# Kernel optimization log

Measured on AMD Instinct MI355X. Metric: run time of the kernel, lower is better.

The kernel has to match this reference:

```python
import jax, jax.numpy as jnp
import numpy as np

HEAD_DIM = 64
NUM_Q_HEADS = 32
NUM_KV_HEADS = 8
ROPE_FREQ = 10000.0
EPS = 1e-6


def _rms_norm(x, gamma):
    # normalize over last dim (head_dim)
    var = jnp.mean(jnp.square(x), axis=-1, keepdims=True)
    return x * jax.lax.rsqrt(var + EPS) * gamma


def _rope_cos_sin(seq_len, dtype=jnp.float32):
    inv_freq = 1.0 / (ROPE_FREQ ** (jnp.arange(0, HEAD_DIM, 2, dtype=jnp.float32) / HEAD_DIM))
    pos = jnp.arange(seq_len, dtype=jnp.float32)
    freqs = pos[:, None] * inv_freq[None, :]          # [S, hd/2]
    emb = jnp.concatenate([freqs, freqs], axis=-1)    # [S, hd]
    return jnp.cos(emb).astype(dtype), jnp.sin(emb).astype(dtype)


def _rotate_half(x):
    x1, x2 = jnp.split(x, 2, axis=-1)
    return jnp.concatenate([-x2, x1], axis=-1)


def _apply_rope(x, cos, sin):
    # x: [B, H, S, hd]; cos/sin: [S, hd]
    return x * cos[None, None, :, :] + _rotate_half(x) * sin[None, None, :, :]


def setup_inputs() -> dict:
    key = jax.random.key(0)
    ks = jax.random.split(key, 5)
    B, S, D = 2, 2048, 2048
    qkv_out = (NUM_Q_HEADS + 2 * NUM_KV_HEADS) * HEAD_DIM  # 3072
    x = jax.random.normal(ks[0], (B, S, D), dtype=jnp.float32)
    w_qkv = jax.random.normal(ks[1], (qkv_out, D), dtype=jnp.float32) * (D ** -0.5)
    w_out = jax.random.normal(ks[2], (D, NUM_Q_HEADS * HEAD_DIM), dtype=jnp.float32) * ((NUM_Q_HEADS * HEAD_DIM) ** -0.5)
    q_gamma = jnp.ones((HEAD_DIM,), dtype=jnp.float32)
    k_gamma = jnp.ones((HEAD_DIM,), dtype=jnp.float32)
    return {"x": x, "w_qkv": w_qkv, "w_out": w_out, "q_gamma": q_gamma, "k_gamma": k_gamma}


def reference(x, w_qkv, w_out, q_gamma, k_gamma):
    B, S, D = x.shape
    groups = NUM_Q_HEADS // NUM_KV_HEADS
    # fused QKV projection (no bias)
    qkv = jnp.einsum("bsd,od->bso", x, w_qkv)
    qkv = qkv.reshape(B, S, NUM_Q_HEADS + 2 * NUM_KV_HEADS, HEAD_DIM)
    qkv = jnp.transpose(qkv, (0, 2, 1, 3))  # [B, heads, S, hd]
    q = qkv[:, :NUM_Q_HEADS]
    k = qkv[:, NUM_Q_HEADS:NUM_Q_HEADS + NUM_KV_HEADS]
    v = qkv[:, NUM_Q_HEADS + NUM_KV_HEADS:]
    # QK RMSNorm over head_dim
    q = _rms_norm(q, q_gamma)
    k = _rms_norm(k, k_gamma)
    # RoPE
    cos, sin = _rope_cos_sin(S, dtype=x.dtype)
    q = _apply_rope(q, cos, sin)
    k = _apply_rope(k, cos, sin)
    # GQA: repeat-interleave kv heads
    k = jnp.repeat(k, groups, axis=1)
    v = jnp.repeat(v, groups, axis=1)
    # causal SDPA
    scale = HEAD_DIM ** -0.5
    scores = jnp.einsum("bhqd,bhkd->bhqk", q, k) * scale
    causal = jnp.tril(jnp.ones((S, S), dtype=bool))
    scores = jnp.where(causal[None, None], scores, jnp.finfo(scores.dtype).min)
    attn = jax.nn.softmax(scores, axis=-1)
    ctx = jnp.einsum("bhqk,bhkd->bhqd", attn, v)
    ctx = jnp.transpose(ctx, (0, 2, 1, 3)).reshape(B, S, NUM_Q_HEADS * HEAD_DIM)
    out = jnp.einsum("bsf,df->bsd", ctx, w_out)
    return out
```

## Files before the change

### kernel.cpp

```cpp
#include <hip/hip_runtime.h>

typedef _Float16 f16;
typedef __fp16 fp16x2 __attribute__((ext_vector_type(2)));
typedef _Float16 f16x8 __attribute__((ext_vector_type(8)));
typedef float f32x4 __attribute__((ext_vector_type(4)));
typedef float f32x16 __attribute__((ext_vector_type(16)));

#define AS1 __attribute__((address_space(1)))
#define AS3 __attribute__((address_space(3)))

#define SCALE_L2E 0.18033688011112042f


__device__ __forceinline__ void gload16(const void* g, void* l) {
    __builtin_amdgcn_global_load_lds(
        (const AS1 unsigned*)(unsigned long long)g,
        (AS3 unsigned*)(unsigned)(unsigned long long)l,
        16, 0, 0);
}

__device__ __forceinline__ unsigned pk2(float a, float b) {
    union { fp16x2 v; unsigned u; } c;
    c.v = __builtin_amdgcn_cvt_pkrtz(a, b);
    return c.u;
}

#define BAR() do { asm volatile("" ::: "memory"); __builtin_amdgcn_s_barrier(); asm volatile("" ::: "memory"); } while (0)


__global__ __launch_bounds__(256) void k_cast(const float* __restrict__ in,
                                              f16* __restrict__ out, int n) {
    int i = (blockIdx.x * 256 + threadIdx.x) * 4;
    if (i + 3 < n) {
        float4 v = *(const float4*)(in + i);
        union { f16 h[4]; ushort4 u; } c;
        c.h[0] = (f16)v.x; c.h[1] = (f16)v.y; c.h[2] = (f16)v.z; c.h[3] = (f16)v.w;
        *(ushort4*)(out + i) = c.u;
    }
}


__global__ __launch_bounds__(256) void k_tab(float* __restrict__ cosT,
                                             float* __restrict__ sinT) {
    int idx = blockIdx.x * 256 + threadIdx.x;
    int s = idx >> 5, i = idx & 31;
    float ang = (float)s * exp2f(-(float)i * 0.4152410118609190f);
    cosT[idx] = cosf(ang);
    sinT[idx] = sinf(ang);
}


#define STG_A(t, h) do { \
    gload16(gA + (size_t)((h) * 128) * K + (t) * 64,      sm + (((t) & 1) * 65536) + (h) * 16384 + tid * 16); \
    gload16(gA + (size_t)((h) * 128 + 64) * K + (t) * 64, sm + (((t) & 1) * 65536) + (h) * 16384 + 8192 + tid * 16); \
} while (0)
#define STG_B(t, h) do { \
    gload16(gB + (size_t)((h) * 128) * K + (t) * 64,      sm + (((t) & 1) * 65536) + 32768 + (h) * 16384 + tid * 16); \
    gload16(gB + (size_t)((h) * 128 + 64) * K + (t) * 64, sm + (((t) & 1) * 65536) + 32768 + (h) * 16384 + 8192 + tid * 16); \
} while (0)

template <typename OutT>
__global__ __launch_bounds__(512, 2) void k_gemm256(const f16* __restrict__ A,
                                                    const f16* __restrict__ Bt,
                                                    OutT* __restrict__ C,
                                                    int M, int N, int K) {
    __shared__ __align__(16) char sm[131072];
    const int tid = threadIdx.x;
    const int lane = tid & 63, wid = tid >> 6;
    const int wm = wid >> 2, wn = wid & 3;
    const int lr = lane & 15, g4 = lane >> 4;
    const int m0 = blockIdx.y * 256, n0 = blockIdx.x * 256;
    const int NT = K >> 6;

    const int srow = tid >> 3;
    const int scol = ((tid & 7) ^ (srow & 7)) * 8;
    const f16* gA = A  + (size_t)(m0 + srow) * K + scol;
    const f16* gB = Bt + (size_t)(n0 + srow) * K + scol;

    f32x4 acc[8][4] = {};
    f16x8 bfr[4][2];

    STG_A(0, 0); STG_A(0, 1); STG_B(0, 0); STG_B(0, 1);
    STG_A(1, 0); STG_A(1, 1); STG_B(1, 0); STG_B(1, 1);
    asm volatile("s_waitcnt vmcnt(8)" ::: "memory");
    BAR();

    for (int t = 0; t < NT; ++t) {
        const int buf = t & 1;
        const char* bA = sm + buf * 65536 + wm * 16384;
        const char* bB = sm + buf * 65536 + 32768 + (wn >> 1) * 16384;
        const bool sA = (t >= 1) && (t + 1 < NT);
        const bool sB = (t + 2 < NT);
#pragma unroll
        for (int p = 0; p < 4; ++p) {
            f16x8 afr[2][2];
            if (p == 0) {
#pragma unroll
                for (int n = 0; n < 4; n++) {
                    const int r = (wn & 1) * 64 + n * 16 + lr;
#pragma unroll
                    for (int kk = 0; kk < 2; kk++)
                        bfr[n][kk] = *(const f16x8*)(bB + ((r * 128 + kk * 64 + g4 * 16) ^ ((r & 7) << 4)));
                }
            }
#pragma unroll
            for (int mm = 0; mm < 2; mm++) {
                const int r = (2 * p + mm) * 16 + lr;
#pragma unroll
                for (int kk = 0; kk < 2; kk++)
                    afr[mm][kk] = *(const f16x8*)(bA + ((r * 128 + kk * 64 + g4 * 16) ^ ((r & 7) << 4)));
            }
            if (p == 0 && sA) STG_A(t + 1, 0);
            if (p == 1 && sA) STG_A(t + 1, 1);
            if (p == 2 && sB) STG_B(t + 2, 0);
            if (p == 3 && sB) STG_B(t + 2, 1);
            BAR();
            asm volatile("s_waitcnt lgkmcnt(0)" ::: "memory");
            __builtin_amdgcn_s_setprio(1);
#pragma unroll
            for (int mm = 0; mm < 2; mm++)
#pragma unroll
                for (int n = 0; n < 4; n++) {
                    acc[2 * p + mm][n] = __builtin_amdgcn_mfma_f32_16x16x32_f16(afr[mm][0], bfr[n][0], acc[2 * p + mm][n], 0, 0, 0);
                    acc[2 * p + mm][n] = __builtin_amdgcn_mfma_f32_16x16x32_f16(afr[mm][1], bfr[n][1], acc[2 * p + mm][n], 0, 0, 0);
                }
            __builtin_amdgcn_s_setprio(0);
            if (p == 3 && t + 1 < NT) {
                if (t + 2 < NT) asm volatile("s_waitcnt vmcnt(4)" ::: "memory");
                else            asm volatile("s_waitcnt vmcnt(0)" ::: "memory");
            }
            BAR();
        }
    }

#pragma unroll
    for (int m = 0; m < 8; m++)
#pragma unroll
        for (int n = 0; n < 4; n++) {
            size_t base = (size_t)(m0 + wm * 128 + m * 16 + g4 * 4) * N + (n0 + wn * 64 + n * 16 + lr);
#pragma unroll
            for (int j = 0; j < 4; j++)
                C[base + (size_t)j * N] = (OutT)acc[m][n][j];
        }
}


__global__ __launch_bounds__(256) void k_qkv_post(const f16* __restrict__ qkv,
                                                  const float* __restrict__ qg,
                                                  const float* __restrict__ kg,
                                                  const float* __restrict__ cosT,
                                                  const float* __restrict__ sinT,
                                                  f16* __restrict__ Qf,
                                                  f16* __restrict__ Kf,
                                                  f16* __restrict__ Vf) {
    __shared__ f16 tl[4][8][72];
    const int tid = threadIdx.x, lane = tid & 63, wv = tid >> 6;
    const int gw = blockIdx.x * 4 + wv;
    const int b = gw / 12288;
    const int r0 = gw - b * 12288;
    const int head = r0 >> 8;
    const int sblk = r0 & 255;
    const int s0 = sblk * 8;
    const int s_loc = lane >> 3, ch = lane & 7;
    const int s = s0 + s_loc;

    f16x8 v = *(const f16x8*)&qkv[((size_t)b * 2048 + s) * 3072 + head * 64 + ch * 8];

    if (head < 40) {
        float vf[8];
#pragma unroll
        for (int j = 0; j < 8; j++) vf[j] = (float)v[j];
        float ss = 0.f;
#pragma unroll
        for (int j = 0; j < 8; j++) ss += vf[j] * vf[j];
        ss += __shfl_xor(ss, 1); ss += __shfl_xor(ss, 2); ss += __shfl_xor(ss, 4);
        float rinv = rsqrtf(ss * (1.0f / 64.0f) + 1e-6f);
        const float* gam = (head < 32 ? qg : kg) + ch * 8;
        float4 g0 = *(const float4*)gam, g1 = *(const float4*)(gam + 4);
        float gv[8] = {g0.x, g0.y, g0.z, g0.w, g1.x, g1.y, g1.z, g1.w};
        float xn[8], ot[8];
#pragma unroll
        for (int j = 0; j < 8; j++) xn[j] = vf[j] * rinv * gv[j];
#pragma unroll
        for (int j = 0; j < 8; j++) ot[j] = __shfl_xor(xn[j], 4);
        const int i0 = (ch & 3) * 8;
        float4 c0  = *(const float4*)&cosT[(s << 5) + i0];
        float4 c1  = *(const float4*)&cosT[(s << 5) + i0 + 4];
        float4 sn0 = *(const float4*)&sinT[(s << 5) + i0];
        float4 sn1 = *(const float4*)&sinT[(s << 5) + i0 + 4];
        float cs[8] = {c0.x, c0.y, c0.z, c0.w, c1.x, c1.y, c1.z, c1.w};
        float sn[8] = {sn0.x, sn0.y, sn0.z, sn0.w, sn1.x, sn1.y, sn1.z, sn1.w};
        float sgn = (ch < 4) ? -1.0f : 1.0f;
        uint4 o;
        o.x = pk2(xn[0]*cs[0] + sgn*ot[0]*sn[0], xn[1]*cs[1] + sgn*ot[1]*sn[1]);
        o.y = pk2(xn[2]*cs[2] + sgn*ot[2]*sn[2], xn[3]*cs[3] + sgn*ot[3]*sn[3]);
        o.z = pk2(xn[4]*cs[4] + sgn*ot[4]*sn[4], xn[5]*cs[5] + sgn*ot[5]*sn[5]);
        o.w = pk2(xn[6]*cs[6] + sgn*ot[6]*sn[6], xn[7]*cs[7] + sgn*ot[7]*sn[7]);
        const int t = s >> 5;
        const int lane2 = (s & 31) + ((ch & 1) << 5);
        const int c = ch >> 1;
        f16* dst = (head < 32)
            ? Qf + (((size_t)(b * 32 + head) * 256 + t * 4 + c) * 512 + lane2 * 8)
            : Kf + (((size_t)(b * 8 + head - 32) * 256 + t * 4 + c) * 512 + lane2 * 8);
        *(uint4*)dst = o;
    } else {
        const int kh = head - 40;
        *(f16x8*)&tl[wv][s_loc][ch * 8] = v;
        asm volatile("s_waitcnt lgkmcnt(0)" ::: "memory");
        f16x8 cv;
#pragma unroll
        for (int rr = 0; rr < 8; rr++) cv[rr] = tl[wv][rr][lane];
        const int d = lane, dh = d >> 5;
        const int t = s0 >> 5, c = (s0 >> 4) & 1, hv = (s0 >> 3) & 1;
        const int g = dh * 2 + c;
        f16* dst = Vf + (((size_t)(b * 8 + kh) * 256 + t * 4 + g) * 512
                         + ((d & 31) + (hv << 5)) * 8);
        *(f16x8*)dst = cv;
    }
}


struct AttnPart { f32x16 o0, o1; float m, l; };

__device__ __forceinline__ AttnPart attn_part(int qb, int par, int lane, int lq, int hi,
        const f16* __restrict__ Qfp, const f16* __restrict__ Kfp,
        const f16* __restrict__ Vfp) {
    f16x8 qf[4];
#pragma unroll
    for (int c = 0; c < 4; c++)
        qf[c] = *(const f16x8*)&Qfp[((size_t)qb * 4 + c) * 512 + lane * 8];

    AttnPart P;
    P.o0 = (f32x16){}; P.o1 = (f32x16){};
    float mrun = -1e30f, lrun = 0.0f;

    f16x8 kf[4];
    if (par <= qb) {
#pragma unroll
        for (int c = 0; c < 4; c++)
            kf[c] = *(const f16x8*)&Kfp[((size_t)par * 4 + c) * 512 + lane * 8];
    }

    for (int kt = par; kt <= qb; kt += 2) {
        f32x16 st = {};
#pragma unroll
        for (int c = 0; c < 4; c++)
            st = __builtin_amdgcn_mfma_f32_32x32x16_f16(kf[c], qf[c], st, 0, 0, 0);

        f16x8 v0[2], v1[2];
#pragma unroll
        for (int c = 0; c < 2; c++) {
            v0[c] = *(const f16x8*)&Vfp[((size_t)kt * 4 + c)     * 512 + lane * 8];
            v1[c] = *(const f16x8*)&Vfp[((size_t)kt * 4 + 2 + c) * 512 + lane * 8];
        }
        if (kt + 2 <= qb) {
#pragma unroll
            for (int c = 0; c < 4; c++)
                kf[c] = *(const f16x8*)&Kfp[((size_t)(kt + 2) * 4 + c) * 512 + lane * 8];
        }

        float tmax = -1e30f;
        if (kt == qb) {
#pragma unroll
            for (int r = 0; r < 16; r++) {
                int kvl = (r & 3) + ((r >> 2) << 3) + (hi << 2);
                float v = (kvl > lq) ? -1e30f : st[r] * SCALE_L2E;
                st[r] = v;
                tmax = fmaxf(tmax, v);
            }
        } else {
#pragma unroll
            for (int r = 0; r < 16; r++) {
                float v = st[r] * SCALE_L2E;
                st[r] = v;
                tmax = fmaxf(tmax, v);
            }
        }
        tmax = fmaxf(tmax, __shfl_xor(tmax, 32));

        if (__any(tmax > mrun + 8.0f)) {
            float mnew  = fmaxf(mrun, tmax);
            float alpha = __builtin_amdgcn_exp2f(mrun - mnew);
            mrun = mnew;
            lrun *= alpha;
            P.o0 = P.o0 * alpha;
            P.o1 = P.o1 * alpha;
        }

        unsigned pkd[8];
        float ps0 = 0.0f, ps1 = 0.0f;
#pragma unroll
        for (int j = 0; j < 8; j++) {
            float p0 = __builtin_amdgcn_exp2f(st[2 * j]     - mrun);
            float p1 = __builtin_amdgcn_exp2f(st[2 * j + 1] - mrun);
            ps0 += p0; ps1 += p1;
            pkd[j] = pk2(p0, p1);
        }
        lrun += ps0 + ps1;

        unsigned oth[8];
#pragma unroll
        for (int j = 0; j < 8; j++) oth[j] = __shfl_xor(pkd[j], 32);

#pragma unroll
        for (int c = 0; c < 2; c++) {
            unsigned m0_ = hi ? pkd[4 * c + 2] : pkd[4 * c];
            unsigned m1_ = hi ? pkd[4 * c + 3] : pkd[4 * c + 1];
            unsigned t0_ = hi ? oth[4 * c + 2] : oth[4 * c];
            unsigned t1_ = hi ? oth[4 * c + 3] : oth[4 * c + 1];
            union { unsigned u[4]; f16x8 v; } pb;
            pb.u[0] = hi ? t0_ : m0_;
            pb.u[1] = hi ? t1_ : m1_;
            pb.u[2] = hi ? m0_ : t0_;
            pb.u[3] = hi ? m1_ : t1_;
            P.o0 = __builtin_amdgcn_mfma_f32_32x32x16_f16(v0[c], pb.v, P.o0, 0, 0, 0);
            P.o1 = __builtin_amdgcn_mfma_f32_32x32x16_f16(v1[c], pb.v, P.o1, 0, 0, 0);
        }
    }

    P.m = mrun;
    P.l = lrun + __shfl_xor(lrun, 32);
    return P;
}

__global__ __launch_bounds__(256) void k_attn(const f16* __restrict__ Qf,
                                              const f16* __restrict__ Kf,
                                              const f16* __restrict__ Vf,
                                              f16* __restrict__ ctx) {
    __shared__ float ldsO[2][32][65];
    __shared__ float ldsM[2][32][2];
    const int wid = threadIdx.x >> 6, lane = threadIdx.x & 63;
    const int lq = lane & 31, hi = lane >> 5;
    const int pairid = wid >> 1, par = wid & 1;
    const int bh = blockIdx.y, b = bh >> 5, h = bh & 31, kh = h >> 2;
    const int pj = blockIdx.x * 2 + pairid;

    const f16* Qfp = Qf + (size_t)(b * 32 + h) * 131072;
    const f16* Kfp = Kf + (size_t)(b * 8 + kh) * 131072;
    const f16* Vfp = Vf + (size_t)(b * 8 + kh) * 131072;
    f16*       ctxbase = ctx + (size_t)b * 2048 * 2048 + h * 64;

    const int qbs[2] = {pj, 63 - pj};
#pragma unroll
    for (int s = 0; s < 2; s++) {
        const int qb = qbs[s];
        AttnPart P = attn_part(qb, par, lane, lq, hi, Qfp, Kfp, Vfp);

        if (par == 1) {
            if (hi == 0) {
                ldsM[pairid][lq][0] = P.m;
                ldsM[pairid][lq][1] = P.l;
            }
#pragma unroll
            for (int r = 0; r < 16; r++) {
                int d = (r & 3) + ((r >> 2) << 3) + (hi << 2);
                ldsO[pairid][lq][d]      = P.o0[r];
                ldsO[pairid][lq][d + 32] = P.o1[r];
            }
        }
        __syncthreads();
        if (par == 0) {
            float m1 = ldsM[pairid][lq][0];
            float l1 = ldsM[pairid][lq][1];
            float M  = fmaxf(P.m, m1);
            float a0 = __builtin_amdgcn_exp2f(P.m - M);
            float a1 = __builtin_amdgcn_exp2f(m1  - M);
            float lc = a0 * P.l + a1 * l1;
            float s0 = a0 / lc, s1 = a1 / lc;
            unsigned* row = (unsigned*)(ctxbase + (size_t)(qb * 32 + lq) * 2048);
#pragma unroll
            for (int g = 0; g < 4; g++) {
                int d = 8 * g + 4 * hi;
                float c0 = P.o0[4 * g]     * s0 + ldsO[pairid][lq][d]     * s1;
                float c1 = P.o0[4 * g + 1] * s0 + ldsO[pairid][lq][d + 1] * s1;
                float c2 = P.o0[4 * g + 2] * s0 + ldsO[pairid][lq][d + 2] * s1;
                float c3 = P.o0[4 * g + 3] * s0 + ldsO[pairid][lq][d + 3] * s1;
                uint2 a; a.x = pk2(c0, c1); a.y = pk2(c2, c3);
                *(uint2*)(row + 2 * hi + 4 * g) = a;
                float e0 = P.o1[4 * g]     * s0 + ldsO[pairid][lq][d + 32] * s1;
                float e1 = P.o1[4 * g + 1] * s0 + ldsO[pairid][lq][d + 33] * s1;
                float e2 = P.o1[4 * g + 2] * s0 + ldsO[pairid][lq][d + 34] * s1;
                float e3 = P.o1[4 * g + 3] * s0 + ldsO[pairid][lq][d + 35] * s1;
                uint2 e; e.x = pk2(e0, e1); e.y = pk2(e2, e3);
                *(uint2*)(row + 16 + 2 * hi + 4 * g) = e;
            }
        }
        __syncthreads();
    }
}


extern "C" void kernel_launch(void* const* d_in, const int* in_sizes, int n_in,
                              void* d_out, int out_size, void* d_ws, size_t ws_size,
                              hipStream_t stream) {
    const float* x     = (const float*)d_in[0];
    const float* w_qkv = (const float*)d_in[1];
    const float* w_out = (const float*)d_in[2];
    const float* qg    = (const float*)d_in[3];
    const float* kg    = (const float*)d_in[4];
    float* out = (float*)d_out;
    char* ws = (char*)d_ws;

    float* cosT = (float*)(ws);
    float* sinT = (float*)(ws + 262144);
    f16* Xh     = (f16*)(ws + 524288);
    f16* Wqkvh  = (f16*)(ws + 17301504);
    f16* Wouth  = (f16*)(ws + 29884416);
    f16* QKVh   = (f16*)(ws + 38273024);
    f16* Qfb    = (f16*)(ws + 63438848);
    f16* Kfb    = (f16*)(ws + 80216064);
    f16* Vfb    = (f16*)(ws + 84410368);
    f16* Ctxh   = (f16*)(ws + 88604672);

    k_cast<<<8388608 / 1024, 256, 0, stream>>>(x, Xh, 8388608);
    k_cast<<<6291456 / 1024, 256, 0, stream>>>(w_qkv, Wqkvh, 6291456);
    k_cast<<<4194304 / 1024, 256, 0, stream>>>(w_out, Wouth, 4194304);
    k_tab<<<256, 256, 0, stream>>>(cosT, sinT);

    k_gemm256<f16><<<dim3(3072 / 256, 4096 / 256), 512, 0, stream>>>(Xh, Wqkvh, QKVh, 4096, 3072, 2048);

    k_qkv_post<<<6144, 256, 0, stream>>>(QKVh, qg, kg, cosT, sinT, Qfb, Kfb, Vfb);

    k_attn<<<dim3(16, 64), 256, 0, stream>>>(Qfb, Kfb, Vfb, Ctxh);

    k_gemm256<float><<<dim3(2048 / 256, 4096 / 256), 512, 0, stream>>>(Ctxh, Wouth, out, 4096, 2048, 2048);
}
```

Before: 220.0 us.

## Fuse casts, fold softmax scale into Q, use permlane swap, retile output GEMM

Merges the three fp16 cast launches into one kernel. Folds the softmax scale times log2(e) into Q during the post-projection step, which removes a multiply per score in attention and shortens the max reduction with three-input max. Replaces the shuffle-based P repack with v_permlane32_swap and shrinks attention blocks to one wave pair each, giving more blocks. Templates the GEMM so the output projection uses a 256x128 tile, which doubles its block count for better CU coverage at the cost of lower per-block reuse.

```diff
diff --git a/kernel.cpp b/kernel.cpp
--- a/kernel.cpp
+++ b/kernel.cpp
@@ -25,18 +25,28 @@
     return c.u;
 }
 
+__device__ __forceinline__ float f3(float a, float b, float c) {
+    return fmaxf(fmaxf(a, b), c);
+}
+
 #define BAR() do { asm volatile("" ::: "memory"); __builtin_amdgcn_s_barrier(); asm volatile("" ::: "memory"); } while (0)
 
 
-__global__ __launch_bounds__(256) void k_cast(const float* __restrict__ in,
-                                              f16* __restrict__ out, int n) {
+__global__ __launch_bounds__(256) void k_cast_all(const float* __restrict__ x,
+                                                  const float* __restrict__ wq,
+                                                  const float* __restrict__ wo,
+                                                  f16* __restrict__ Xh,
+                                                  f16* __restrict__ Wqh,
+                                                  f16* __restrict__ Woh) {
     int i = (blockIdx.x * 256 + threadIdx.x) * 4;
-    if (i + 3 < n) {
-        float4 v = *(const float4*)(in + i);
-        union { f16 h[4]; ushort4 u; } c;
-        c.h[0] = (f16)v.x; c.h[1] = (f16)v.y; c.h[2] = (f16)v.z; c.h[3] = (f16)v.w;
-        *(ushort4*)(out + i) = c.u;
-    }
+    const float* src; f16* dst;
+    if (i < 8388608)        { src = x  + i;            dst = Xh  + i; }
+    else if (i < 14680064)  { src = wq + (i - 8388608); dst = Wqh + (i - 8388608); }
+    else                    { src = wo + (i - 14680064); dst = Woh + (i - 14680064); }
+    float4 v = *(const float4*)src;
+    union { f16 h[4]; ushort4 u; } c;
+    c.h[0] = (f16)v.x; c.h[1] = (f16)v.y; c.h[2] = (f16)v.z; c.h[3] = (f16)v.w;
+    *(ushort4*)dst = c.u;
 }
 
 
@@ -50,26 +60,19 @@
 }
 
 
-#define STG_A(t, h) do { \
-    gload16(gA + (size_t)((h) * 128) * K + (t) * 64,      sm + (((t) & 1) * 65536) + (h) * 16384 + tid * 16); \
-    gload16(gA + (size_t)((h) * 128 + 64) * K + (t) * 64, sm + (((t) & 1) * 65536) + (h) * 16384 + 8192 + tid * 16); \
-} while (0)
-#define STG_B(t, h) do { \
-    gload16(gB + (size_t)((h) * 128) * K + (t) * 64,      sm + (((t) & 1) * 65536) + 32768 + (h) * 16384 + tid * 16); \
-    gload16(gB + (size_t)((h) * 128 + 64) * K + (t) * 64, sm + (((t) & 1) * 65536) + 32768 + (h) * 16384 + 8192 + tid * 16); \
-} while (0)
-
-template <typename OutT>
+template <typename OutT, int BH>
 __global__ __launch_bounds__(512, 2) void k_gemm256(const f16* __restrict__ A,
                                                     const f16* __restrict__ Bt,
                                                     OutT* __restrict__ C,
                                                     int M, int N, int K) {
-    __shared__ __align__(16) char sm[131072];
+    constexpr int BUFSZ = 32768 + BH * 16384;
+    constexpr int NN = 2 * BH;
+    __shared__ __align__(16) char sm[2 * BUFSZ];
     const int tid = threadIdx.x;
     const int lane = tid & 63, wid = tid >> 6;
     const int wm = wid >> 2, wn = wid & 3;
     const int lr = lane & 15, g4 = lane >> 4;
-    const int m0 = blockIdx.y * 256, n0 = blockIdx.x * 256;
+    const int m0 = blockIdx.y * 256, n0 = blockIdx.x * (128 * BH);
     const int NT = K >> 6;
 
     const int srow = tid >> 3;
@@ -77,18 +80,30 @@
     const f16* gA = A  + (size_t)(m0 + srow) * K + scol;
     const f16* gB = Bt + (size_t)(n0 + srow) * K + scol;
 
-    f32x4 acc[8][4] = {};
-    f16x8 bfr[4][2];
-
-    STG_A(0, 0); STG_A(0, 1); STG_B(0, 0); STG_B(0, 1);
-    STG_A(1, 0); STG_A(1, 1); STG_B(1, 0); STG_B(1, 1);
-    asm volatile("s_waitcnt vmcnt(8)" ::: "memory");
+    auto STGA = [&](int t, int h) {
+        char* d = sm + (t & 1) * BUFSZ + h * 16384 + tid * 16;
+        gload16(gA + (size_t)(h * 128) * K + t * 64,      d);
+        gload16(gA + (size_t)(h * 128 + 64) * K + t * 64, d + 8192);
+    };
+    auto STGB = [&](int t, int h) {
+        char* d = sm + (t & 1) * BUFSZ + 32768 + h * 16384 + tid * 16;
+        gload16(gB + (size_t)(h * 128) * K + t * 64,      d);
+        gload16(gB + (size_t)(h * 128 + 64) * K + t * 64, d + 8192);
+    };
+
+    f32x4 acc[8][NN] = {};
+    f16x8 bfr[NN][2];
+
+    STGA(0, 0); STGA(0, 1); STGB(0, 0); if (BH == 2) STGB(0, 1);
+    STGA(1, 0); STGA(1, 1); STGB(1, 0); if (BH == 2) STGB(1, 1);
+    if constexpr (BH == 2) asm volatile("s_waitcnt vmcnt(8)" ::: "memory");
+    else                   asm volatile("s_waitcnt vmcnt(6)" ::: "memory");
     BAR();
 
     for (int t = 0; t < NT; ++t) {
         const int buf = t & 1;
-        const char* bA = sm + buf * 65536 + wm * 16384;
-        const char* bB = sm + buf * 65536 + 32768 + (wn >> 1) * 16384;
+        const char* bA = sm + buf * BUFSZ + wm * 16384;
+        const char* bB = sm + buf * BUFSZ + 32768 + (BH == 2 ? (wn >> 1) * 16384 : 0);
         const bool sA = (t >= 1) && (t + 1 < NT);
         const bool sB = (t + 2 < NT);
 #pragma unroll
@@ -96,8 +111,8 @@
             f16x8 afr[2][2];
             if (p == 0) {
 #pragma unroll
-                for (int n = 0; n < 4; n++) {
-                    const int r = (wn & 1) * 64 + n * 16 + lr;
+                for (int n = 0; n < NN; n++) {
+                    const int r = (BH == 2 ? (wn & 1) * 64 : wn * 32) + n * 16 + lr;
 #pragma unroll
                     for (int kk = 0; kk < 2; kk++)
                         bfr[n][kk] = *(const f16x8*)(bB + ((r * 128 + kk * 64 + g4 * 16) ^ ((r & 7) << 4)));
@@ -110,24 +125,28 @@
                 for (int kk = 0; kk < 2; kk++)
                     afr[mm][kk] = *(const f16x8*)(bA + ((r * 128 + kk * 64 + g4 * 16) ^ ((r & 7) << 4)));
             }
-            if (p == 0 && sA) STG_A(t + 1, 0);
-            if (p == 1 && sA) STG_A(t + 1, 1);
-            if (p == 2 && sB) STG_B(t + 2, 0);
-            if (p == 3 && sB) STG_B(t + 2, 1);
+            if (p == 0 && sA) STGA(t + 1, 0);
+            if (p == 1 && sA) STGA(t + 1, 1);
+            if (p == 2 && sB) STGB(t + 2, 0);
+            if (p == 3 && sB && BH == 2) STGB(t + 2, 1);
             BAR();
             asm volatile("s_waitcnt lgkmcnt(0)" ::: "memory");
             __builtin_amdgcn_s_setprio(1);
 #pragma unroll
             for (int mm = 0; mm < 2; mm++)
 #pragma unroll
-                for (int n = 0; n < 4; n++) {
+                for (int n = 0; n < NN; n++) {
                     acc[2 * p + mm][n] = __builtin_amdgcn_mfma_f32_16x16x32_f16(afr[mm][0], bfr[n][0], acc[2 * p + mm][n], 0, 0, 0);
                     acc[2 * p + mm][n] = __builtin_amdgcn_mfma_f32_16x16x32_f16(afr[mm][1], bfr[n][1], acc[2 * p + mm][n], 0, 0, 0);
                 }
             __builtin_amdgcn_s_setprio(0);
             if (p == 3 && t + 1 < NT) {
-                if (t + 2 < NT) asm volatile("s_waitcnt vmcnt(4)" ::: "memory");
-                else            asm volatile("s_waitcnt vmcnt(0)" ::: "memory");
+                if (t + 2 < NT) {
+                    if constexpr (BH == 2) asm volatile("s_waitcnt vmcnt(4)" ::: "memory");
+                    else                   asm volatile("s_waitcnt vmcnt(2)" ::: "memory");
+                } else {
+                    asm volatile("s_waitcnt vmcnt(0)" ::: "memory");
+                }
             }
             BAR();
         }
@@ -136,8 +155,8 @@
 #pragma unroll
     for (int m = 0; m < 8; m++)
 #pragma unroll
-        for (int n = 0; n < 4; n++) {
-            size_t base = (size_t)(m0 + wm * 128 + m * 16 + g4 * 4) * N + (n0 + wn * 64 + n * 16 + lr);
+        for (int n = 0; n < NN; n++) {
+            size_t base = (size_t)(m0 + wm * 128 + m * 16 + g4 * 4) * N + (n0 + wn * (32 * BH) + n * 16 + lr);
 #pragma unroll
             for (int j = 0; j < 4; j++)
                 C[base + (size_t)j * N] = (OutT)acc[m][n][j];
@@ -191,11 +210,16 @@
         float cs[8] = {c0.x, c0.y, c0.z, c0.w, c1.x, c1.y, c1.z, c1.w};
         float sn[8] = {sn0.x, sn0.y, sn0.z, sn0.w, sn1.x, sn1.y, sn1.z, sn1.w};
         float sgn = (ch < 4) ? -1.0f : 1.0f;
+        float ov[8];
+#pragma unroll
+        for (int j = 0; j < 8; j++) ov[j] = xn[j] * cs[j] + sgn * ot[j] * sn[j];
+        if (head < 32) {
+#pragma unroll
+            for (int j = 0; j < 8; j++) ov[j] *= SCALE_L2E;
+        }
         uint4 o;
-        o.x = pk2(xn[0]*cs[0] + sgn*ot[0]*sn[0], xn[1]*cs[1] + sgn*ot[1]*sn[1]);
-        o.y = pk2(xn[2]*cs[2] + sgn*ot[2]*sn[2], xn[3]*cs[3] + sgn*ot[3]*sn[3]);
-        o.z = pk2(xn[4]*cs[4] + sgn*ot[4]*sn[4], xn[5]*cs[5] + sgn*ot[5]*sn[5]);
-        o.w = pk2(xn[6]*cs[6] + sgn*ot[6]*sn[6], xn[7]*cs[7] + sgn*ot[7]*sn[7]);
+        o.x = pk2(ov[0], ov[1]); o.y = pk2(ov[2], ov[3]);
+        o.z = pk2(ov[4], ov[5]); o.w = pk2(ov[6], ov[7]);
         const int t = s >> 5;
         const int lane2 = (s & 31) + ((ch & 1) << 5);
         const int c = ch >> 1;
@@ -259,23 +283,19 @@
                 kf[c] = *(const f16x8*)&Kfp[((size_t)(kt + 2) * 4 + c) * 512 + lane * 8];
         }
 
-        float tmax = -1e30f;
         if (kt == qb) {
 #pragma unroll
             for (int r = 0; r < 16; r++) {
                 int kvl = (r & 3) + ((r >> 2) << 3) + (hi << 2);
-                float v = (kvl > lq) ? -1e30f : st[r] * SCALE_L2E;
-                st[r] = v;
-                tmax = fmaxf(tmax, v);
-            }
-        } else {
-#pragma unroll
-            for (int r = 0; r < 16; r++) {
-                float v = st[r] * SCALE_L2E;
-                st[r] = v;
-                tmax = fmaxf(tmax, v);
-            }
-        }
+                if (kvl > lq) st[r] = -1e30f;
+            }
+        }
+        float t0 = f3(st[0],  st[1],  st[2]);
+        float t1 = f3(st[3],  st[4],  st[5]);
+        float t2 = f3(st[6],  st[7],  st[8]);
+        float t3 = f3(st[9],  st[10], st[11]);
+        float t4 = f3(st[12], st[13], st[14]);
+        float tmax = fmaxf(f3(t0, t1, t2), f3(t3, t4, st[15]));
         tmax = fmaxf(tmax, __shfl_xor(tmax, 32));
 
         if (__any(tmax > mrun + 8.0f)) {
@@ -287,32 +307,24 @@
             P.o1 = P.o1 * alpha;
         }
 
-        unsigned pkd[8];
+        unsigned X[8];
         float ps0 = 0.0f, ps1 = 0.0f;
 #pragma unroll
         for (int j = 0; j < 8; j++) {
             float p0 = __builtin_amdgcn_exp2f(st[2 * j]     - mrun);
             float p1 = __builtin_amdgcn_exp2f(st[2 * j + 1] - mrun);
             ps0 += p0; ps1 += p1;
-            pkd[j] = pk2(p0, p1);
+            X[j] = pk2(p0, p1);
         }
         lrun += ps0 + ps1;
 
-        unsigned oth[8];
-#pragma unroll
-        for (int j = 0; j < 8; j++) oth[j] = __shfl_xor(pkd[j], 32);
-
 #pragma unroll
         for (int c = 0; c < 2; c++) {
-            unsigned m0_ = hi ? pkd[4 * c + 2] : pkd[4 * c];
-            unsigned m1_ = hi ? pkd[4 * c + 3] : pkd[4 * c + 1];
-            unsigned t0_ = hi ? oth[4 * c + 2] : oth[4 * c];
-            unsigned t1_ = hi ? oth[4 * c + 3] : oth[4 * c + 1];
+            unsigned a0 = X[4 * c], a1 = X[4 * c + 1], a2 = X[4 * c + 2], a3 = X[4 * c + 3];
+            asm volatile("v_permlane32_swap_b32 %0, %1" : "+v"(a0), "+v"(a2));
+            asm volatile("v_permlane32_swap_b32 %0, %1" : "+v"(a1), "+v"(a3));
             union { unsigned u[4]; f16x8 v; } pb;
-            pb.u[0] = hi ? t0_ : m0_;
-            pb.u[1] = hi ? t1_ : m1_;
-            pb.u[2] = hi ? m0_ : t0_;
-            pb.u[3] = hi ? m1_ : t1_;
+            pb.u[0] = a0; pb.u[1] = a1; pb.u[2] = a2; pb.u[3] = a3;
             P.o0 = __builtin_amdgcn_mfma_f32_32x32x16_f16(v0[c], pb.v, P.o0, 0, 0, 0);
             P.o1 = __builtin_amdgcn_mfma_f32_32x32x16_f16(v1[c], pb.v, P.o1, 0, 0, 0);
         }
@@ -323,17 +335,17 @@
     return P;
 }
 
-__global__ __launch_bounds__(256) void k_attn(const f16* __restrict__ Qf,
+__global__ __launch_bounds__(128) void k_attn(const f16* __restrict__ Qf,
                                               const f16* __restrict__ Kf,
                                               const f16* __restrict__ Vf,
                                               f16* __restrict__ ctx) {
-    __shared__ float ldsO[2][32][65];
-    __shared__ float ldsM[2][32][2];
-    const int wid = threadIdx.x >> 6, lane = threadIdx.x & 63;
+    __shared__ float ldsO[32][65];
+    __shared__ float ldsM[32][2];
+    const int tid = threadIdx.x;
+    const int par = tid >> 6, lane = tid & 63;
     const int lq = lane & 31, hi = lane >> 5;
-    const int pairid = wid >> 1, par = wid & 1;
     const int bh = blockIdx.y, b = bh >> 5, h = bh & 31, kh = h >> 2;
-    const int pj = blockIdx.x * 2 + pairid;
+    const int pj = blockIdx.x;
 
     const f16* Qfp = Qf + (size_t)(b * 32 + h) * 131072;
     const f16* Kfp = Kf + (size_t)(b * 8 + kh) * 131072;
@@ -348,20 +360,20 @@
 
         if (par == 1) {
             if (hi == 0) {
-                ldsM[pairid][lq][0] = P.m;
-                ldsM[pairid][lq][1] = P.l;
+                ldsM[lq][0] = P.m;
+                ldsM[lq][1] = P.l;
             }
 #pragma unroll
             for (int r = 0; r < 16; r++) {
                 int d = (r & 3) + ((r >> 2) << 3) + (hi << 2);
-                ldsO[pairid][lq][d]      = P.o0[r];
-                ldsO[pairid][lq][d + 32] = P.o1[r];
+                ldsO[lq][d]      = P.o0[r];
+                ldsO[lq][d + 32] = P.o1[r];
             }
         }
         __syncthreads();
         if (par == 0) {
-            float m1 = ldsM[pairid][lq][0];
-            float l1 = ldsM[pairid][lq][1];
+            float m1 = ldsM[lq][0];
+            float l1 = ldsM[lq][1];
             float M  = fmaxf(P.m, m1);
             float a0 = __builtin_amdgcn_exp2f(P.m - M);
             float a1 = __builtin_amdgcn_exp2f(m1  - M);
@@ -371,16 +383,16 @@
 #pragma unroll
             for (int g = 0; g < 4; g++) {
                 int d = 8 * g + 4 * hi;
-                float c0 = P.o0[4 * g]     * s0 + ldsO[pairid][lq][d]     * s1;
-                float c1 = P.o0[4 * g + 1] * s0 + ldsO[pairid][lq][d + 1] * s1;
-                float c2 = P.o0[4 * g + 2] * s0 + ldsO[pairid][lq][d + 2] * s1;
-                float c3 = P.o0[4 * g + 3] * s0 + ldsO[pairid][lq][d + 3] * s1;
+                float c0 = P.o0[4 * g]     * s0 + ldsO[lq][d]     * s1;
+                float c1 = P.o0[4 * g + 1] * s0 + ldsO[lq][d + 1] * s1;
+                float c2 = P.o0[4 * g + 2] * s0 + ldsO[lq][d + 2] * s1;
+                float c3 = P.o0[4 * g + 3] * s0 + ldsO[lq][d + 3] * s1;
                 uint2 a; a.x = pk2(c0, c1); a.y = pk2(c2, c3);
                 *(uint2*)(row + 2 * hi + 4 * g) = a;
-                float e0 = P.o1[4 * g]     * s0 + ldsO[pairid][lq][d + 32] * s1;
-                float e1 = P.o1[4 * g + 1] * s0 + ldsO[pairid][lq][d + 33] * s1;
-                float e2 = P.o1[4 * g + 2] * s0 + ldsO[pairid][lq][d + 34] * s1;
-                float e3 = P.o1[4 * g + 3] * s0 + ldsO[pairid][lq][d + 35] * s1;
+                float e0 = P.o1[4 * g]     * s0 + ldsO[lq][d + 32] * s1;
+                float e1 = P.o1[4 * g + 1] * s0 + ldsO[lq][d + 33] * s1;
+                float e2 = P.o1[4 * g + 2] * s0 + ldsO[lq][d + 34] * s1;
+                float e3 = P.o1[4 * g + 3] * s0 + ldsO[lq][d + 35] * s1;
                 uint2 e; e.x = pk2(e0, e1); e.y = pk2(e2, e3);
                 *(uint2*)(row + 16 + 2 * hi + 4 * g) = e;
             }
@@ -412,16 +424,14 @@
     f16* Vfb    = (f16*)(ws + 84410368);
     f16* Ctxh   = (f16*)(ws + 88604672);
 
-    k_cast<<<8388608 / 1024, 256, 0, stream>>>(x, Xh, 8388608);
-    k_cast<<<6291456 / 1024, 256, 0, stream>>>(w_qkv, Wqkvh, 6291456);
-    k_cast<<<4194304 / 1024, 256, 0, stream>>>(w_out, Wouth, 4194304);
+    k_cast_all<<<18432, 256, 0, stream>>>(x, w_qkv, w_out, Xh, Wqkvh, Wouth);
     k_tab<<<256, 256, 0, stream>>>(cosT, sinT);
 
-    k_gemm256<f16><<<dim3(3072 / 256, 4096 / 256), 512, 0, stream>>>(Xh, Wqkvh, QKVh, 4096, 3072, 2048);
+    k_gemm256<f16, 2><<<dim3(12, 16), 512, 0, stream>>>(Xh, Wqkvh, QKVh, 4096, 3072, 2048);
 
     k_qkv_post<<<6144, 256, 0, stream>>>(QKVh, qg, kg, cosT, sinT, Qfb, Kfb, Vfb);
 
-    k_attn<<<dim3(16, 64), 256, 0, stream>>>(Qfb, Kfb, Vfb, Ctxh);
-
-    k_gemm256<float><<<dim3(2048 / 256, 4096 / 256), 512, 0, stream>>>(Ctxh, Wouth, out, 4096, 2048, 2048);
-}
+    k_attn<<<dim3(32, 64), 128, 0, stream>>>(Qfb, Kfb, Vfb, Ctxh);
+
+    k_gemm256<float, 1><<<dim3(16, 16), 512, 0, stream>>>(Ctxh, Wouth, out, 4096, 2048, 2048);
+}
```

Result: faster. 207.8 us (-5.5%).
